# Kernel tuning notes

Measured on AMD Instinct MI355X. Metric: run time of the kernel, lower is better.

## Reference

```python
import jax, jax.numpy as jnp
import numpy as np

EPS = 1e-5

def layernorm(x, g, b):
    mu = jnp.mean(x, axis=-1, keepdims=True)
    var = jnp.mean((x - mu) ** 2, axis=-1, keepdims=True)
    return (x - mu) * jax.lax.rsqrt(var + EPS) * g + b

def setup_inputs() -> dict:
    key = jax.random.key(0)
    B, T, C, H = 4, 2048, 1024, 16
    hs = C // H  # 64
    ks = jax.random.split(key, 16)
    s_in = 1.0 / np.sqrt(C)
    s_hid = 1.0 / np.sqrt(4 * C)
    return {
        "x":   jax.random.normal(ks[0], (B, T, C), jnp.float32),
        # per-head projections, stacked over heads: [H, C, hs]
        "Wq":  jax.random.normal(ks[1], (H, C, hs), jnp.float32) * s_in,
        "Wk":  jax.random.normal(ks[2], (H, C, hs), jnp.float32) * s_in,
        "Wv":  jax.random.normal(ks[3], (H, C, hs), jnp.float32) * s_in,
        # output projection [C, C] (concat of heads -> C)
        "Wo":  jax.random.normal(ks[4], (C, C), jnp.float32) * s_in,
        "bo":  jnp.zeros((C,), jnp.float32),
        # layernorm params
        "g1":  jnp.ones((C,), jnp.float32),
        "be1": jnp.zeros((C,), jnp.float32),
        "g2":  jnp.ones((C,), jnp.float32),
        "be2": jnp.zeros((C,), jnp.float32),
        # feed-forward: C -> 4C -> C
        "W1":  jax.random.normal(ks[5], (C, 4 * C), jnp.float32) * s_in,
        "b1":  jnp.zeros((4 * C,), jnp.float32),
        "W2":  jax.random.normal(ks[6], (4 * C, C), jnp.float32) * s_hid,
        "b2":  jnp.zeros((C,), jnp.float32),
    }

def reference(x, Wq, Wk, Wv, Wo, bo, g1, be1, g2, be2, W1, b1, W2, b2):
    B, T, C = x.shape
    H, _, hs = Wq.shape
    scale = hs ** -0.5

    # --- self-attention on ln1(x) ---
    xn = layernorm(x, g1, be1)
    q = jnp.einsum('btc,hcd->bhtd', xn, Wq)
    k = jnp.einsum('btc,hcd->bhtd', xn, Wk)
    v = jnp.einsum('btc,hcd->bhtd', xn, Wv)
    scores = jnp.einsum('bhtd,bhsd->bhts', q, k) * scale  # [B,H,T,T]
    causal = jnp.tril(jnp.ones((T, T), dtype=bool))
    scores = jnp.where(causal, scores, jnp.finfo(scores.dtype).min)
    wei = jax.nn.softmax(scores, axis=-1)
    out = jnp.einsum('bhts,bhsd->bhtd', wei, v)           # [B,H,T,hs]
    out = out.transpose(0, 2, 1, 3).reshape(B, T, H * hs)  # concat heads
    x = x + out @ Wo + bo

    # --- feed-forward on ln2(x) ---
    xn2 = layernorm(x, g2, be2)
    h = jax.nn.relu(xn2 @ W1 + b1)
    x = x + h @ W2 + b2
    return x
```

## Files before the change

kernel.cpp:

```cpp
#include <hip/hip_runtime.h>
#include <hip/hip_bf16.h>

typedef __hip_bfloat16 bf16;
typedef __attribute__((ext_vector_type(8))) short bf16x8;
typedef __attribute__((ext_vector_type(4))) short s16x4;
typedef __attribute__((ext_vector_type(4))) float f32x4;

__device__ __forceinline__ float b2f(bf16 v) { return __bfloat162float(v); }
__device__ __forceinline__ bf16  f2b(float v) { return __float2bfloat16(v); }
__device__ __forceinline__ float ldf(const bf16* p)  { return __bfloat162float(*p); }
__device__ __forceinline__ float ldf(const float* p) { return *p; }
__device__ __forceinline__ void  stf(bf16* p, float v)  { *p = __float2bfloat16(v); }
__device__ __forceinline__ void  stf(float* p, float v) { *p = v; }

__device__ __forceinline__ void load_lds16(const bf16* g, short* lds) {
    __builtin_amdgcn_global_load_lds(
        (const __attribute__((address_space(1))) unsigned int*)g,
        (__attribute__((address_space(3))) unsigned int*)lds, 16, 0, 0);
}

template<typename InT>
__global__ __launch_bounds__(256) void ln_kernel(const InT* __restrict__ x,
                                                 const float* __restrict__ g,
                                                 const float* __restrict__ b,
                                                 bf16* __restrict__ out)
{
    const int C = 1024;
    int row = blockIdx.x;
    int tid = threadIdx.x;
    const InT* xr = x + (size_t)row * C;

    float v[4];
    float s = 0.f, s2 = 0.f;
#pragma unroll
    for (int i = 0; i < 4; ++i) {
        float f = ldf(xr + tid + i * 256);
        v[i] = f; s += f; s2 += f * f;
    }
#pragma unroll
    for (int off = 32; off > 0; off >>= 1) {
        s  += __shfl_down(s,  off, 64);
        s2 += __shfl_down(s2, off, 64);
    }
    __shared__ float red[8];
    int wave = tid >> 6;
    if ((tid & 63) == 0) { red[wave] = s; red[wave + 4] = s2; }
    __syncthreads();
    float ts  = red[0] + red[1] + red[2] + red[3];
    float ts2 = red[4] + red[5] + red[6] + red[7];
    float mu  = ts * (1.f / 1024.f);
    float var = ts2 * (1.f / 1024.f) - mu * mu;
    float rstd = rsqrtf(var + 1e-5f);
#pragma unroll
    for (int i = 0; i < 4; ++i) {
        int c = tid + i * 256;
        out[(size_t)row * C + c] = f2b((v[i] - mu) * rstd * g[c] + b[c]);
    }
}

__global__ __launch_bounds__(256) void prep_weights(
    const float* __restrict__ Wq, const float* __restrict__ Wk,
    const float* __restrict__ Wv, const float* __restrict__ Wo,
    const float* __restrict__ W1, const float* __restrict__ W2,
    bf16* __restrict__ wqkvt, bf16* __restrict__ wot,
    bf16* __restrict__ w1t, bf16* __restrict__ w2t)
{
    __shared__ float t[32][33];
    int tx = threadIdx.x & 31, ty = threadIdx.x >> 5;
    int id = blockIdx.x;
    const float* in; bf16* out; int in_ld, out_ld, n0, k0;
    if (id < 3072) {
        const float* Ws[3] = {Wq, Wk, Wv};
        int m = id >> 10, r = id & 1023;
        int z = r >> 6, rt = r & 63;
        in = Ws[m] + z * 65536;
        out = wqkvt + (size_t)(m * 1024 + z * 64) * 1024;
        in_ld = 64; out_ld = 1024;
        n0 = (rt & 1) * 32; k0 = (rt >> 1) * 32;
    } else if (id < 4096) {
        int r = id - 3072;
        in = Wo; out = wot; in_ld = 1024; out_ld = 1024;
        n0 = (r & 31) * 32; k0 = (r >> 5) * 32;
    } else if (id < 8192) {
        int r = id - 4096;
        in = W1; out = w1t; in_ld = 4096; out_ld = 1024;
        n0 = (r & 127) * 32; k0 = (r >> 7) * 32;
    } else {
        int r = id - 8192;
        in = W2; out = w2t; in_ld = 1024; out_ld = 4096;
        n0 = (r & 31) * 32; k0 = (r >> 5) * 32;
    }
#pragma unroll
    for (int i = 0; i < 4; ++i)
        t[ty + i * 8][tx] = in[(size_t)(k0 + ty + i * 8) * in_ld + n0 + tx];
    __syncthreads();
#pragma unroll
    for (int i = 0; i < 4; ++i)
        out[(size_t)(n0 + ty + i * 8) * out_ld + k0 + tx] = f2b(t[tx][ty + i * 8]);
}

__global__ __launch_bounds__(256) void vt_kernel(
    const bf16* __restrict__ qkv, bf16* __restrict__ vt, int T)
{
    __shared__ float t[32][33];
    int tx = threadIdx.x & 31, ty = threadIdx.x >> 5;
    int z = blockIdx.z, b = z >> 4, h = z & 15;
    const bf16* in = qkv + (size_t)b * T * 3072 + 2048 + h * 64;
    bf16* out = vt + (size_t)z * 64 * T;
    int n0 = blockIdx.x * 32, k0 = blockIdx.y * 32;
#pragma unroll
    for (int i = 0; i < 4; ++i)
        t[ty + i * 8][tx] = b2f(in[(size_t)(k0 + ty + i * 8) * 3072 + n0 + tx]);
    __syncthreads();
#pragma unroll
    for (int i = 0; i < 4; ++i)
        out[(size_t)(n0 + ty + i * 8) * T + k0 + tx] = f2b(t[tx][ty + i * 8]);
}

template<bool RELU, bool HAS_BIAS, bool HAS_RES, typename ResT, typename OutT>
__global__ __launch_bounds__(256) void gemm_bt(
    const bf16* __restrict__ A, int lda,
    const bf16* __restrict__ Bt, int ldb,
    const float* __restrict__ bias,
    const ResT* __restrict__ res, int ldr,
    OutT* __restrict__ Cm, int ldc,
    int M, int N, int K)
{
    __shared__ short As[2][128 * 32];
    __shared__ short Bs[2][128 * 32];
    int tid = threadIdx.x, wv = tid >> 6, ln = tid & 63;

    int f = blockIdx.x + blockIdx.y * gridDim.x;
    int nby = gridDim.y;
    int by = f % nby, bx = f / nby;
    int bm0 = by * 128, bn0 = bx * 128;

    int wm = (wv & 1) * 64, wn = (wv >> 1) * 64;
    int quad = ln >> 4, lane15 = ln & 15;

    f32x4 acc[4][4] = {};

    int srow = ln >> 2;
    int scol = (((ln & 3) ^ (srow & 3)) * 8);
    int sw   = (quad ^ (lane15 & 3)) * 8;
    const bf16* Ab = A + (size_t)bm0 * lda;
    const bf16* Bb = Bt + (size_t)bn0 * ldb;

#pragma unroll
    for (int i = 0; i < 2; ++i) {
        int ch = wv + i * 4;
        load_lds16(Ab + (size_t)(ch * 16 + srow) * lda + scol, &As[0][ch * 16 * 32]);
        load_lds16(Bb + (size_t)(ch * 16 + srow) * ldb + scol, &Bs[0][ch * 16 * 32]);
    }
    __syncthreads();

    int cur = 0;
    for (int k0 = 0; k0 < K; k0 += 32) {
        if (k0 + 32 < K) {
            int nb = cur ^ 1;
#pragma unroll
            for (int i = 0; i < 2; ++i) {
                int ch = wv + i * 4;
                load_lds16(Ab + (size_t)(ch * 16 + srow) * lda + k0 + 32 + scol,
                           &As[nb][ch * 16 * 32]);
                load_lds16(Bb + (size_t)(ch * 16 + srow) * ldb + k0 + 32 + scol,
                           &Bs[nb][ch * 16 * 32]);
            }
        }
        bf16x8 af[4], bfr[4];
#pragma unroll
        for (int mi = 0; mi < 4; ++mi)
            af[mi] = *(const bf16x8*)&As[cur][(wm + mi * 16 + lane15) * 32 + sw];
#pragma unroll
        for (int ni = 0; ni < 4; ++ni)
            bfr[ni] = *(const bf16x8*)&Bs[cur][(wn + ni * 16 + lane15) * 32 + sw];
#pragma unroll
        for (int mi = 0; mi < 4; ++mi)
#pragma unroll
            for (int ni = 0; ni < 4; ++ni)
                acc[mi][ni] = __builtin_amdgcn_mfma_f32_16x16x32_bf16(
                    af[mi], bfr[ni], acc[mi][ni], 0, 0, 0);
        __syncthreads();
        cur ^= 1;
    }

#pragma unroll
    for (int mi = 0; mi < 4; ++mi) {
#pragma unroll
        for (int r = 0; r < 4; ++r) {
            int gm = bm0 + wm + mi * 16 + quad * 4 + r;
#pragma unroll
            for (int ni = 0; ni < 4; ++ni) {
                int gn = bn0 + wn + ni * 16 + lane15;
                float v = acc[mi][ni][r];
                if (HAS_BIAS) v += bias[gn];
                if (HAS_RES)  v += ldf(res + (size_t)gm * ldr + gn);
                if (RELU)     v = fmaxf(v, 0.f);
                stf(Cm + (size_t)gm * ldc + gn, v);
            }
        }
    }
}

__global__ __launch_bounds__(512) void attn_kernel(
    const bf16* __restrict__ qkv, const bf16* __restrict__ vt,
    bf16* __restrict__ o, int T)
{
    const int LDQ = 3072;
    const int PS = 72;
    int qt = (int)gridDim.x - 1 - (int)blockIdx.x;
    int h = blockIdx.y, b = blockIdx.z;
    int tid = threadIdx.x, wv = tid >> 6, ln = tid & 63;
    int quad = ln >> 4, lane15 = ln & 15, r7 = lane15 & 7;

    __shared__ short KV[2][2][64 * 64];
    __shared__ short Ps[8][16 * PS];

    int lr = ln >> 3;
    int lc = ((ln & 7) ^ lr) * 8;

    const bf16* kbase = qkv + (size_t)(b * T) * LDQ + 1024 + h * 64;
    const bf16* vbase = vt + (size_t)((b * 16 + h) * 64) * T;

    short* Qarea = &KV[0][0][0];
#pragma unroll
    for (int i = 0; i < 2; ++i) {
        int ch = wv * 2 + i;
        load_lds16(qkv + (size_t)(b * T + qt * 128 + ch * 8 + lr) * LDQ + h * 64 + lc,
                   &Qarea[ch * 512]);
    }
    __syncthreads();
    bf16x8 qf[2];
#pragma unroll
    for (int ks = 0; ks < 2; ++ks)
        qf[ks] = *(const bf16x8*)&Qarea[(wv * 16 + lane15) * 64 + (((ks * 4 + quad) ^ r7) * 8)];
    __syncthreads();

    f32x4 oacc[4] = {};
    float mrun = -1e30f, lrun = 0.f;
    const float scale = 0.125f;
    int qmin = qt * 128 + wv * 16;
    int ntiles = 2 * qt + 2;

    load_lds16(kbase + (size_t)(0 * 64 + wv * 8 + lr) * LDQ + lc, &KV[0][0][wv * 8 * 64]);
    load_lds16(vbase + (size_t)(wv * 8 + lr) * T + 0 * 64 + lc, &KV[0][1][wv * 8 * 64]);

    for (int kt = 0; kt < ntiles; ++kt) {
        __syncthreads();
        if (kt + 1 < ntiles) {
            int nb = (kt + 1) & 1;
            load_lds16(kbase + (size_t)((kt + 1) * 64 + wv * 8 + lr) * LDQ + lc,
                       &KV[nb][0][wv * 8 * 64]);
            load_lds16(vbase + (size_t)(wv * 8 + lr) * T + (kt + 1) * 64 + lc,
                       &KV[nb][1][wv * 8 * 64]);
        }
        if (kt * 64 > qmin + 15) continue;

        const short* Ks = &KV[kt & 1][0][0];
        const short* Vs = &KV[kt & 1][1][0];

        f32x4 sacc[4] = {};
        __builtin_amdgcn_s_setprio(1);
#pragma unroll
        for (int ks = 0; ks < 2; ++ks) {
            int so = ((ks * 4 + quad) ^ r7) * 8;
#pragma unroll
            for (int mi = 0; mi < 4; ++mi) {
                bf16x8 kf = *(const bf16x8*)&Ks[(mi * 16 + lane15) * 64 + so];
                sacc[mi] = __builtin_amdgcn_mfma_f32_16x16x32_bf16(kf, qf[ks], sacc[mi], 0, 0, 0);
            }
        }
        __builtin_amdgcn_s_setprio(0);

        if (kt * 64 + 63 > qmin) {
            int ql = qmin + lane15;
#pragma unroll
            for (int mi = 0; mi < 4; ++mi)
#pragma unroll
                for (int r = 0; r < 4; ++r)
                    if (kt * 64 + mi * 16 + quad * 4 + r > ql) sacc[mi][r] = -3e38f;
        }

        float mx = sacc[0][0];
#pragma unroll
        for (int mi = 0; mi < 4; ++mi)
#pragma unroll
            for (int r = 0; r < 4; ++r) mx = fmaxf(mx, sacc[mi][r]);
        mx = fmaxf(mx, __shfl_xor(mx, 16, 64));
        mx = fmaxf(mx, __shfl_xor(mx, 32, 64));
        float pmax = mx * scale;

        if (!__all(pmax <= mrun + 8.f)) {
            float mn = fmaxf(mrun, pmax);
            float alpha = __expf(mrun - mn);
            mrun = mn;
            lrun *= alpha;
#pragma unroll
            for (int di = 0; di < 4; ++di)
#pragma unroll
                for (int r = 0; r < 4; ++r) oacc[di][r] *= alpha;
        }

        float psum = 0.f;
#pragma unroll
        for (int mi = 0; mi < 4; ++mi) {
            float p[4];
#pragma unroll
            for (int r = 0; r < 4; ++r) {
                p[r] = __expf(fmaf(sacc[mi][r], scale, -mrun));
                psum += p[r];
            }
            short tmp[4];
#pragma unroll
            for (int r = 0; r < 4; ++r) {
                bf16 pb = f2b(p[r]);
                tmp[r] = *(short*)&pb;
            }
            *(s16x4*)&Ps[wv][lane15 * PS + mi * 16 + quad * 4] = *(s16x4*)tmp;
        }
        lrun += psum;

        __builtin_amdgcn_s_setprio(1);
#pragma unroll
        for (int ks = 0; ks < 2; ++ks) {
            int so = ((ks * 4 + quad) ^ r7) * 8;
            bf16x8 pf = *(const bf16x8*)&Ps[wv][lane15 * PS + ks * 32 + quad * 8];
#pragma unroll
            for (int di = 0; di < 4; ++di) {
                bf16x8 vf = *(const bf16x8*)&Vs[(di * 16 + lane15) * 64 + so];
                oacc[di] = __builtin_amdgcn_mfma_f32_16x16x32_bf16(vf, pf, oacc[di], 0, 0, 0);
            }
        }
        __builtin_amdgcn_s_setprio(0);
    }

    lrun += __shfl_xor(lrun, 16, 64);
    lrun += __shfl_xor(lrun, 32, 64);
    float inv = 1.f / lrun;

    size_t row = (size_t)(b * T + qt * 128 + wv * 16 + lane15);
#pragma unroll
    for (int di = 0; di < 4; ++di) {
        short tmp[4];
#pragma unroll
        for (int r = 0; r < 4; ++r) {
            bf16 ob = f2b(oacc[di][r] * inv);
            tmp[r] = *(short*)&ob;
        }
        *(s16x4*)&o[row * 1024 + h * 64 + di * 16 + quad * 4] = *(s16x4*)tmp;
    }
}

extern "C" void kernel_launch(void* const* d_in, const int* in_sizes, int n_in,
                              void* d_out, int out_size, void* d_ws, size_t ws_size,
                              hipStream_t stream)
{
    (void)in_sizes; (void)n_in; (void)out_size; (void)ws_size;
    const float* x   = (const float*)d_in[0];
    const float* Wq  = (const float*)d_in[1];
    const float* Wk  = (const float*)d_in[2];
    const float* Wv  = (const float*)d_in[3];
    const float* Wo  = (const float*)d_in[4];
    const float* bo  = (const float*)d_in[5];
    const float* g1  = (const float*)d_in[6];
    const float* be1 = (const float*)d_in[7];
    const float* g2  = (const float*)d_in[8];
    const float* be2 = (const float*)d_in[9];
    const float* W1  = (const float*)d_in[10];
    const float* b1  = (const float*)d_in[11];
    const float* W2  = (const float*)d_in[12];
    const float* b2  = (const float*)d_in[13];

    const int T = 2048, M = 4 * T;
    const size_t MB = 1ull << 20;
    char* ws = (char*)d_ws;

    bf16*  xn    = (bf16*)(ws + 0 * MB);
    bf16*  qkv   = (bf16*)(ws + 16 * MB);
    bf16*  vt    = (bf16*)(ws + 64 * MB);
    bf16*  wqkvt = (bf16*)(ws + 80 * MB);
    bf16*  x1b   = (bf16*)(ws + 80 * MB);
    bf16*  wot   = (bf16*)(ws + 96 * MB);
    bf16*  xn2   = (bf16*)(ws + 96 * MB);
    bf16*  w1t   = (bf16*)(ws + 112 * MB);
    bf16*  w2t   = (bf16*)(ws + 120 * MB);
    bf16*  attnb = (bf16*)(ws + 0 * MB);
    bf16*  hb    = (bf16*)(ws + 0 * MB);

    dim3 blk(256);

    prep_weights<<<12288, blk, 0, stream>>>(Wq, Wk, Wv, Wo, W1, W2,
                                            wqkvt, wot, w1t, w2t);

    ln_kernel<float><<<M, blk, 0, stream>>>(x, g1, be1, xn);

    gemm_bt<false, false, false, float, bf16><<<dim3(24, 64), blk, 0, stream>>>(
        xn, 1024, wqkvt, 1024, nullptr, nullptr, 0, qkv, 3072, M, 3072, 1024);

    vt_kernel<<<dim3(2, T / 32, 64), blk, 0, stream>>>(qkv, vt, T);

    attn_kernel<<<dim3(T / 128, 16, 4), dim3(512), 0, stream>>>(qkv, vt, attnb, T);

    gemm_bt<false, true, true, float, bf16><<<dim3(8, 64), blk, 0, stream>>>(
        attnb, 1024, wot, 1024, bo, x, 1024, x1b, 1024, M, 1024, 1024);

    ln_kernel<bf16><<<M, blk, 0, stream>>>(x1b, g2, be2, xn2);

    gemm_bt<true, true, false, float, bf16><<<dim3(32, 64), blk, 0, stream>>>(
        xn2, 1024, w1t, 1024, b1, nullptr, 0, hb, 4096, M, 4096, 1024);

    gemm_bt<false, true, true, bf16, float><<<dim3(8, 64), blk, 0, stream>>>(
        hb, 4096, w2t, 4096, b2, x1b, 1024, (float*)d_out, 1024, M, 1024, 4096);
}
```

Measured before the change: 534.3 us.

## Pair complementary causal query tiles per attention block to balance work and share K/V

Each attention block now handles two query tiles, qt and 15-qt, so every block does the same amount of causal work and each K/V tile loaded into LDS is reused by both query tiles. The grid shrinks from 16 to 8 blocks along the query axis. The kernel also switches softmax to exp2 with a pre-folded log2e scale, and adds an occupancy hint to launch_bounds. The cost is twice the accumulator registers per thread, which may limit occupancy, and the grid now has only 512 blocks.

```diff
diff --git a/kernel.cpp b/kernel.cpp
--- a/kernel.cpp
+++ b/kernel.cpp
@@ -202,19 +202,104 @@
     }
 }
 
-__global__ __launch_bounds__(512) void attn_kernel(
+__device__ __forceinline__ void attn_tile_q(
+    const short* __restrict__ Ks, const short* __restrict__ Vs,
+    short* __restrict__ Psw,
+    const bf16x8* qf, f32x4* oacc, float& mrun, float& lrun,
+    int ktbase, int qmin, int quad, int lane15, int r7)
+{
+    const float scale2 = 0.18033688011112042f;
+    const int PS = 72;
+    f32x4 sacc[4] = {};
+    __builtin_amdgcn_s_setprio(1);
+#pragma unroll
+    for (int ks = 0; ks < 2; ++ks) {
+        int so = ((ks * 4 + quad) ^ r7) * 8;
+#pragma unroll
+        for (int mi = 0; mi < 4; ++mi) {
+            bf16x8 kf = *(const bf16x8*)&Ks[(mi * 16 + lane15) * 64 + so];
+            sacc[mi] = __builtin_amdgcn_mfma_f32_16x16x32_bf16(kf, qf[ks], sacc[mi], 0, 0, 0);
+        }
+    }
+    __builtin_amdgcn_s_setprio(0);
+
+    if (ktbase + 63 > qmin) {
+        int ql = qmin + lane15;
+#pragma unroll
+        for (int mi = 0; mi < 4; ++mi)
+#pragma unroll
+            for (int r = 0; r < 4; ++r)
+                if (ktbase + mi * 16 + quad * 4 + r > ql) sacc[mi][r] = -3e38f;
+    }
+
+    float mx = sacc[0][0];
+#pragma unroll
+    for (int mi = 0; mi < 4; ++mi)
+#pragma unroll
+        for (int r = 0; r < 4; ++r) mx = fmaxf(mx, sacc[mi][r]);
+    mx = fmaxf(mx, __shfl_xor(mx, 16, 64));
+    mx = fmaxf(mx, __shfl_xor(mx, 32, 64));
+    float pmax = mx * scale2;
+
+    if (!__all(pmax <= mrun + 11.5f)) {
+        float mn = fmaxf(mrun, pmax);
+        float alpha = exp2f(mrun - mn);
+        mrun = mn;
+        lrun *= alpha;
+#pragma unroll
+        for (int di = 0; di < 4; ++di)
+#pragma unroll
+            for (int r = 0; r < 4; ++r) oacc[di][r] *= alpha;
+    }
+
+    float psum = 0.f;
+#pragma unroll
+    for (int mi = 0; mi < 4; ++mi) {
+        float p[4];
+#pragma unroll
+        for (int r = 0; r < 4; ++r) {
+            p[r] = exp2f(fmaf(sacc[mi][r], scale2, -mrun));
+            psum += p[r];
+        }
+        short tmp[4];
+#pragma unroll
+        for (int r = 0; r < 4; ++r) {
+            bf16 pb = f2b(p[r]);
+            tmp[r] = *(short*)&pb;
+        }
+        *(s16x4*)&Psw[lane15 * PS + mi * 16 + quad * 4] = *(s16x4*)tmp;
+    }
+    lrun += psum;
+
+    __builtin_amdgcn_s_setprio(1);
+#pragma unroll
+    for (int ks = 0; ks < 2; ++ks) {
+        int so = ((ks * 4 + quad) ^ r7) * 8;
+        bf16x8 pf = *(const bf16x8*)&Psw[lane15 * PS + ks * 32 + quad * 8];
+#pragma unroll
+        for (int di = 0; di < 4; ++di) {
+            bf16x8 vf = *(const bf16x8*)&Vs[(di * 16 + lane15) * 64 + so];
+            oacc[di] = __builtin_amdgcn_mfma_f32_16x16x32_bf16(vf, pf, oacc[di], 0, 0, 0);
+        }
+    }
+    __builtin_amdgcn_s_setprio(0);
+}
+
+__global__ __launch_bounds__(512, 4) void attn_kernel(
     const bf16* __restrict__ qkv, const bf16* __restrict__ vt,
     bf16* __restrict__ o, int T)
 {
     const int LDQ = 3072;
     const int PS = 72;
-    int qt = (int)gridDim.x - 1 - (int)blockIdx.x;
+    int bx = blockIdx.x;
+    int qta = 15 - bx;
+    int qtb = bx;
     int h = blockIdx.y, b = blockIdx.z;
     int tid = threadIdx.x, wv = tid >> 6, ln = tid & 63;
     int quad = ln >> 4, lane15 = ln & 15, r7 = lane15 & 7;
 
     __shared__ short KV[2][2][64 * 64];
-    __shared__ short Ps[8][16 * PS];
+    __shared__ short Ps[2][8][16 * PS];
 
     int lr = ln >> 3;
     int lc = ((ln & 7) ^ lr) * 8;
@@ -222,28 +307,32 @@
     const bf16* kbase = qkv + (size_t)(b * T) * LDQ + 1024 + h * 64;
     const bf16* vbase = vt + (size_t)((b * 16 + h) * 64) * T;
 
-    short* Qarea = &KV[0][0][0];
 #pragma unroll
     for (int i = 0; i < 2; ++i) {
         int ch = wv * 2 + i;
-        load_lds16(qkv + (size_t)(b * T + qt * 128 + ch * 8 + lr) * LDQ + h * 64 + lc,
-                   &Qarea[ch * 512]);
-    }
-    __syncthreads();
-    bf16x8 qf[2];
-#pragma unroll
-    for (int ks = 0; ks < 2; ++ks)
-        qf[ks] = *(const bf16x8*)&Qarea[(wv * 16 + lane15) * 64 + (((ks * 4 + quad) ^ r7) * 8)];
-    __syncthreads();
-
-    f32x4 oacc[4] = {};
-    float mrun = -1e30f, lrun = 0.f;
-    const float scale = 0.125f;
-    int qmin = qt * 128 + wv * 16;
-    int ntiles = 2 * qt + 2;
-
-    load_lds16(kbase + (size_t)(0 * 64 + wv * 8 + lr) * LDQ + lc, &KV[0][0][wv * 8 * 64]);
-    load_lds16(vbase + (size_t)(wv * 8 + lr) * T + 0 * 64 + lc, &KV[0][1][wv * 8 * 64]);
+        load_lds16(qkv + (size_t)(b * T + qta * 128 + ch * 8 + lr) * LDQ + h * 64 + lc,
+                   &KV[0][0][ch * 512]);
+        load_lds16(qkv + (size_t)(b * T + qtb * 128 + ch * 8 + lr) * LDQ + h * 64 + lc,
+                   &KV[1][0][ch * 512]);
+    }
+    __syncthreads();
+    bf16x8 qfa[2], qfb[2];
+#pragma unroll
+    for (int ks = 0; ks < 2; ++ks) {
+        int off = (wv * 16 + lane15) * 64 + (((ks * 4 + quad) ^ r7) * 8);
+        qfa[ks] = *(const bf16x8*)&KV[0][0][off];
+        qfb[ks] = *(const bf16x8*)&KV[1][0][off];
+    }
+    __syncthreads();
+
+    f32x4 oacca[4] = {}, oaccb[4] = {};
+    float mra = -1e30f, lra = 0.f, mrb = -1e30f, lrb = 0.f;
+    int qmina = qta * 128 + wv * 16;
+    int qminb = qtb * 128 + wv * 16;
+    int ntiles = 2 * qta + 2;
+
+    load_lds16(kbase + (size_t)(wv * 8 + lr) * LDQ + lc, &KV[0][0][wv * 8 * 64]);
+    load_lds16(vbase + (size_t)(wv * 8 + lr) * T + lc, &KV[0][1][wv * 8 * 64]);
 
     for (int kt = 0; kt < ntiles; ++kt) {
         __syncthreads();
@@ -254,100 +343,46 @@
             load_lds16(vbase + (size_t)(wv * 8 + lr) * T + (kt + 1) * 64 + lc,
                        &KV[nb][1][wv * 8 * 64]);
         }
-        if (kt * 64 > qmin + 15) continue;
-
         const short* Ks = &KV[kt & 1][0][0];
         const short* Vs = &KV[kt & 1][1][0];
-
-        f32x4 sacc[4] = {};
-        __builtin_amdgcn_s_setprio(1);
-#pragma unroll
-        for (int ks = 0; ks < 2; ++ks) {
-            int so = ((ks * 4 + quad) ^ r7) * 8;
-#pragma unroll
-            for (int mi = 0; mi < 4; ++mi) {
-                bf16x8 kf = *(const bf16x8*)&Ks[(mi * 16 + lane15) * 64 + so];
-                sacc[mi] = __builtin_amdgcn_mfma_f32_16x16x32_bf16(kf, qf[ks], sacc[mi], 0, 0, 0);
-            }
-        }
-        __builtin_amdgcn_s_setprio(0);
-
-        if (kt * 64 + 63 > qmin) {
-            int ql = qmin + lane15;
-#pragma unroll
-            for (int mi = 0; mi < 4; ++mi)
-#pragma unroll
-                for (int r = 0; r < 4; ++r)
-                    if (kt * 64 + mi * 16 + quad * 4 + r > ql) sacc[mi][r] = -3e38f;
-        }
-
-        float mx = sacc[0][0];
-#pragma unroll
-        for (int mi = 0; mi < 4; ++mi)
-#pragma unroll
-            for (int r = 0; r < 4; ++r) mx = fmaxf(mx, sacc[mi][r]);
-        mx = fmaxf(mx, __shfl_xor(mx, 16, 64));
-        mx = fmaxf(mx, __shfl_xor(mx, 32, 64));
-        float pmax = mx * scale;
-
-        if (!__all(pmax <= mrun + 8.f)) {
-            float mn = fmaxf(mrun, pmax);
-            float alpha = __expf(mrun - mn);
-            mrun = mn;
-            lrun *= alpha;
-#pragma unroll
-            for (int di = 0; di < 4; ++di)
-#pragma unroll
-                for (int r = 0; r < 4; ++r) oacc[di][r] *= alpha;
-        }
-
-        float psum = 0.f;
-#pragma unroll
-        for (int mi = 0; mi < 4; ++mi) {
-            float p[4];
-#pragma unroll
-            for (int r = 0; r < 4; ++r) {
-                p[r] = __expf(fmaf(sacc[mi][r], scale, -mrun));
-                psum += p[r];
-            }
-            short tmp[4];
-#pragma unroll
-            for (int r = 0; r < 4; ++r) {
-                bf16 pb = f2b(p[r]);
-                tmp[r] = *(short*)&pb;
-            }
-            *(s16x4*)&Ps[wv][lane15 * PS + mi * 16 + quad * 4] = *(s16x4*)tmp;
-        }
-        lrun += psum;
-
-        __builtin_amdgcn_s_setprio(1);
-#pragma unroll
-        for (int ks = 0; ks < 2; ++ks) {
-            int so = ((ks * 4 + quad) ^ r7) * 8;
-            bf16x8 pf = *(const bf16x8*)&Ps[wv][lane15 * PS + ks * 32 + quad * 8];
-#pragma unroll
-            for (int di = 0; di < 4; ++di) {
-                bf16x8 vf = *(const bf16x8*)&Vs[(di * 16 + lane15) * 64 + so];
-                oacc[di] = __builtin_amdgcn_mfma_f32_16x16x32_bf16(vf, pf, oacc[di], 0, 0, 0);
-            }
-        }
-        __builtin_amdgcn_s_setprio(0);
-    }
-
-    lrun += __shfl_xor(lrun, 16, 64);
-    lrun += __shfl_xor(lrun, 32, 64);
-    float inv = 1.f / lrun;
-
-    size_t row = (size_t)(b * T + qt * 128 + wv * 16 + lane15);
+        int kb = kt * 64;
+
+        if (kb <= qmina + 15)
+            attn_tile_q(Ks, Vs, &Ps[0][wv][0], qfa, oacca, mra, lra,
+                        kb, qmina, quad, lane15, r7);
+        if (kb <= qminb + 15)
+            attn_tile_q(Ks, Vs, &Ps[1][wv][0], qfb, oaccb, mrb, lrb,
+                        kb, qminb, quad, lane15, r7);
+    }
+
+    lra += __shfl_xor(lra, 16, 64);
+    lra += __shfl_xor(lra, 32, 64);
+    float inva = 1.f / lra;
+    size_t rowa = (size_t)(b * T + qta * 128 + wv * 16 + lane15);
 #pragma unroll
     for (int di = 0; di < 4; ++di) {
         short tmp[4];
 #pragma unroll
         for (int r = 0; r < 4; ++r) {
-            bf16 ob = f2b(oacc[di][r] * inv);
+            bf16 ob = f2b(oacca[di][r] * inva);
             tmp[r] = *(short*)&ob;
         }
-        *(s16x4*)&o[row * 1024 + h * 64 + di * 16 + quad * 4] = *(s16x4*)tmp;
+        *(s16x4*)&o[rowa * 1024 + h * 64 + di * 16 + quad * 4] = *(s16x4*)tmp;
+    }
+
+    lrb += __shfl_xor(lrb, 16, 64);
+    lrb += __shfl_xor(lrb, 32, 64);
+    float invb = 1.f / lrb;
+    size_t rowb = (size_t)(b * T + qtb * 128 + wv * 16 + lane15);
+#pragma unroll
+    for (int di = 0; di < 4; ++di) {
+        short tmp[4];
+#pragma unroll
+        for (int r = 0; r < 4; ++r) {
+            bf16 ob = f2b(oaccb[di][r] * invb);
+            tmp[r] = *(short*)&ob;
+        }
+        *(s16x4*)&o[rowb * 1024 + h * 64 + di * 16 + quad * 4] = *(s16x4*)tmp;
     }
 }
 
@@ -399,7 +434,7 @@
 
     vt_kernel<<<dim3(2, T / 32, 64), blk, 0, stream>>>(qkv, vt, T);
 
-    attn_kernel<<<dim3(T / 128, 16, 4), dim3(512), 0, stream>>>(qkv, vt, attnb, T);
+    attn_kernel<<<dim3(8, 16, 4), dim3(512), 0, stream>>>(qkv, vt, attnb, T);
 
     gemm_bt<false, true, true, float, bf16><<<dim3(8, 64), blk, 0, stream>>>(
         attnb, 1024, wot, 1024, bo, x, 1024, x1b, 1024, M, 1024, 1024);
```

Result: faster. 504.8 us (-5.5%).
